# Kernel tuning notes

Measured on AMD Instinct MI355X. Metric: run time of the kernel, lower is better.

## Reference

```python
import jax, jax.numpy as jnp
import numpy as np
import math

B, S, HID = 4, 2048, 1024
H, D = 16, HID // 16


def setup_inputs() -> dict:
    key = jax.random.key(0)
    ks = jax.random.split(key, 6)
    scale = 0.02
    inp = {
        "hidden_states": jax.random.normal(ks[0], (B, S, HID), dtype=jnp.float32),
        "Wq": jax.random.normal(ks[1], (HID, HID), dtype=jnp.float32) * scale,
        "bq": jnp.zeros((HID,), dtype=jnp.float32),
        "Wk1": jax.random.normal(ks[2], (HID, HID), dtype=jnp.float32) * scale,
        "bk1": jnp.zeros((HID,), dtype=jnp.float32),
        "Wk2": jax.random.normal(ks[3], (HID, HID), dtype=jnp.float32) * scale,
        "bk2": jnp.zeros((HID,), dtype=jnp.float32),
        "Wv1": jax.random.normal(ks[4], (HID, HID), dtype=jnp.float32) * scale,
        "bv1": jnp.zeros((HID,), dtype=jnp.float32),
        "Wv2": jax.random.normal(ks[5], (HID, HID), dtype=jnp.float32) * scale,
        "bv2": jnp.zeros((HID,), dtype=jnp.float32),
    }
    return inp


def _heads(x):
    # [B, S, HID] -> [B, H, S, D]
    return x.reshape(B, S, H, D).transpose(0, 2, 1, 3)


def reference(hidden_states, Wq, bq, Wk1, bk1, Wk2, bk2, Wv1, bv1, Wv2, bv2):
    # nn.Linear uses y = x @ W^T + b
    q = _heads(hidden_states @ Wq.T + bq)
    k1 = _heads(hidden_states @ Wk1.T + bk1)
    k2 = _heads(hidden_states @ Wk2.T + bk2)
    v1 = _heads(hidden_states @ Wv1.T + bv1)
    v2 = _heads(hidden_states @ Wv2.T + bv2)

    inv_sqrt_d = 1.0 / math.sqrt(D)
    scores = jnp.einsum('bhqd,bhkd->bhqk', q, k1) * inv_sqrt_d  # [B,H,S,S]
    probs = jax.nn.softmax(scores, axis=-1)
    ctx = jnp.einsum('bhqk,bhkd->bhqd', probs, v1)              # [B,H,S,D]
    ctx = jnp.einsum('bhqd,bhkd->bhqk', ctx, k2)                # [B,H,S,S]
    ctx = jnp.einsum('bhqk,bhkd->bhqd', ctx, v2)                # [B,H,S,D]
    # [B,H,S,D] -> [B,S,HID]
    return ctx.transpose(0, 2, 1, 3).reshape(B, S, HID)
```

## Files before the change

### kernel.cpp

```cpp
#include <hip/hip_runtime.h>
#include <hip/hip_bf16.h>

#define HIDD 1024
#define BATCH 4
#define SEQ 2048
#define NHEAD 16
#define HD 64
#define NW 5
#define MROWS (BATCH*SEQ)
#define NCOLS (NW*HIDD)

typedef __attribute__((ext_vector_type(8))) short bf16x8;
typedef __attribute__((ext_vector_type(4))) float f32x4;
typedef __attribute__((ext_vector_type(16))) float f32x16;
typedef __attribute__((ext_vector_type(4))) unsigned int uint4v;

__device__ __forceinline__ unsigned short f2b(float f) {
    __hip_bfloat16 h = __float2bfloat16(f);
    return __builtin_bit_cast(unsigned short, h);
}
__device__ __forceinline__ float b2f(unsigned short u) {
    __hip_bfloat16 h = __builtin_bit_cast(__hip_bfloat16, u);
    return __bfloat162float(h);
}

#if __has_builtin(__builtin_amdgcn_exp2f)
#define EXP2(x) __builtin_amdgcn_exp2f(x)
#else
#define EXP2(x) exp2f(x)
#endif

typedef __attribute__((address_space(1))) const void gvoid;
typedef __attribute__((address_space(3))) void lvoid;
__device__ __forceinline__ void gload16(const void* src, void* dst) {
    __builtin_amdgcn_global_load_lds((gvoid*)src, (lvoid*)dst, 16, 0, 0);
}

__global__ void cvt_kernel(const float* __restrict__ X,
                           const float* __restrict__ W0, const float* __restrict__ W1,
                           const float* __restrict__ W2, const float* __restrict__ W3,
                           const float* __restrict__ W4,
                           unsigned short* __restrict__ Xb, unsigned short* __restrict__ Wb)
{
    const int XN = MROWS * HIDD / 4;
    const int WN = HIDD * HIDD / 4;
    int i = blockIdx.x * 256 + threadIdx.x;
    if (i >= XN + 5 * WN) return;
    const float* src; unsigned short* dst; int off;
    if (i < XN) { src = X; dst = Xb; off = i; }
    else {
        int j = i - XN; int w = j / WN; int r = j - w * WN;
        src = (w == 0 ? W0 : w == 1 ? W1 : w == 2 ? W2 : w == 3 ? W3 : W4);
        dst = Wb + (long)w * HIDD * HIDD; off = r;
    }
    float4 v = ((const float4*)src)[off];
    short4 o;
    o.x = (short)f2b(v.x); o.y = (short)f2b(v.y);
    o.z = (short)f2b(v.z); o.w = (short)f2b(v.w);
    ((short4*)dst)[off] = o;
}

#define READ_A(buf, kh, mh) \
    _Pragma("unroll") \
    for (int mt = 0; mt < 4; ++mt) \
        af[mt] = *(const bf16x8*)((const char*)As[buf][kh] + \
                  (wr * 128 + (mh) * 64 + mt * 16 + q) * 64 + ((g ^ csw) << 4));
#define READ_B(buf, kh) \
    _Pragma("unroll") \
    for (int nt = 0; nt < 4; ++nt) \
        bfr[nt] = *(const bf16x8*)((const char*)Bs[buf][kh] + \
                  (wc * 64 + nt * 16 + q) * 64 + ((g ^ csw) << 4));
#define MFMA_Q(mh) \
    asm volatile("s_waitcnt lgkmcnt(0)" ::: "memory"); \
    __builtin_amdgcn_sched_barrier(0); \
    __builtin_amdgcn_s_setprio(1); \
    _Pragma("unroll") \
    for (int mt = 0; mt < 4; ++mt) \
    _Pragma("unroll") \
    for (int nt = 0; nt < 4; ++nt) \
        acc[(mh) * 4 + mt][nt] = __builtin_amdgcn_mfma_f32_16x16x32_bf16( \
            af[mt], bfr[nt], acc[(mh) * 4 + mt][nt], 0, 0, 0); \
    __builtin_amdgcn_s_setprio(0);

__global__ __launch_bounds__(512, 2) void gemm_proj(
    const unsigned short* __restrict__ Xb, const unsigned short* __restrict__ Wb,
    const float* __restrict__ pb0, const float* __restrict__ pb1, const float* __restrict__ pb2,
    const float* __restrict__ pb3, const float* __restrict__ pb4,
    unsigned short* __restrict__ C)
{
    __shared__ __align__(16) unsigned short As[2][2][256 * 32];
    __shared__ __align__(16) unsigned short Bs[2][2][256 * 32];
    int tid = threadIdx.x;
    int n = blockIdx.x;
    int xcd = n & 7, op = n >> 3;
    int ntile = (op < 16) ? 2 : 1;
    int lane = tid & 63, w = tid >> 6;
    int wr = w >> 2, wc = w & 3;
    int q = lane & 15, g = lane >> 4;
    int csw = (q >> 1) & 3;
    int srow = tid >> 2;
    int scol = ((tid & 3) ^ ((tid >> 3) & 3)) * 8;

    for (int tix = 0; tix < ntile; ++tix) {
        int o = op + tix * 64;
        int bm = xcd * 4 + (o & 3);
        int bn = o >> 2;

        if (tix) { asm volatile("s_barrier" ::: "memory"); }

        f32x4 acc[8][4] = {};
        const unsigned short* Ag = Xb + (long)(bm * 256) * HIDD;
        const unsigned short* Bg = Wb + (long)(bn * 256) * HIDD;

        auto stage = [&](const unsigned short* G, unsigned short* slot, int kc) {
#pragma unroll
            for (int l = 0; l < 2; ++l)
                gload16(G + (long)(l * 128 + srow) * HIDD + kc + scol,
                        (char*)slot + (l * 512 + tid) * 16);
        };

        stage(Ag, As[0][0], 0);
        stage(Bg, Bs[0][0], 0);
        stage(Ag, As[0][1], 32);
        stage(Bg, Bs[0][1], 32);
        stage(Ag, As[1][0], 64);
        stage(Bg, Bs[1][0], 64);

        for (int t = 0; t < 16; ++t) {
            int buf = t & 1;
            int kc1 = ((t + 1) & 15) * 64;
            int kc2 = ((t + 2) & 15) * 64;
            bf16x8 af[4], bfr[4];
            asm volatile("s_waitcnt vmcnt(8)" ::: "memory");
            asm volatile("s_barrier" ::: "memory");
            READ_A(buf, 0, 0)
            READ_B(buf, 0)
            stage(Ag, As[buf ^ 1][1], kc1 + 32);
            MFMA_Q(0)
            READ_A(buf, 0, 1)
            stage(Bg, Bs[buf ^ 1][1], kc1 + 32);
            MFMA_Q(1)
            asm volatile("s_waitcnt vmcnt(8)" ::: "memory");
            asm volatile("s_barrier" ::: "memory");
            READ_A(buf, 1, 0)
            READ_B(buf, 1)
            stage(Ag, As[buf][0], kc2);
            MFMA_Q(0)
            READ_A(buf, 1, 1)
            stage(Bg, Bs[buf][0], kc2);
            MFMA_Q(1)
        }

        int ncol0 = bn * 256 + wc * 64 + q;
        const float* bp = (bn < 4 ? pb0 : bn < 8 ? pb1 : bn < 12 ? pb2 : bn < 16 ? pb3 : pb4);
#pragma unroll
        for (int nt = 0; nt < 4; ++nt) {
            int ncol = ncol0 + nt * 16;
            float bv = bp[ncol & 1023];
#pragma unroll
            for (int mt = 0; mt < 8; ++mt) {
                int row = bm * 256 + wr * 128 + mt * 16 + g * 4;
#pragma unroll
                for (int r = 0; r < 4; ++r)
                    C[(long)(row + r) * NCOLS + ncol] = f2b(acc[mt][nt][r] + bv);
            }
        }
    }
}

#define QSCALE 0.180336880f
#define LDV 72
#define NT (SEQ / 64)

__global__ __launch_bounds__(512, 2) void flash1(
    const unsigned short* __restrict__ C, unsigned short* __restrict__ ctx)
{
    __shared__ unsigned short Ks[2][64 * 64];
    __shared__ unsigned short Vs[2][64 * LDV];
    __shared__ float Lbuf[8][32];
    int tid = threadIdx.x;
    int lane = tid & 63, w = tid >> 6;
    int q32 = lane & 31, hi = lane >> 5;
    int n = blockIdx.x;
    int qt = (n >> 3) & 7;
    int bh = (n & 7) * 8 + (n >> 6);
    int b = bh >> 4, h = bh & 15;
    long rowbase = (long)(b * SEQ) * NCOLS;
    int s0 = qt * 256;

    const unsigned short* Kg = C + rowbase + 1 * HIDD + h * 64;
    const unsigned short* Vg = C + rowbase + 3 * HIDD + h * 64;

    int krlo = lane >> 3;
    int kch  = (lane & 7) ^ krlo;
    int kp = tid & 31, dc = tid >> 5;
    int rsw = q32 & 7;

    bf16x8 qreg[4];
    {
        const unsigned short* Qp = C + rowbase + (long)(s0 + w * 32 + q32) * NCOLS + h * 64;
#pragma unroll
        for (int s = 0; s < 4; ++s) {
            bf16x8 v = *(const bf16x8*)(Qp + s * 16 + hi * 8);
#pragma unroll
            for (int j = 0; j < 8; j++)
                v[j] = (short)f2b(b2f((unsigned short)v[j]) * QSCALE);
            qreg[s] = v;
        }
    }

    gload16(Kg + (long)(w * 8 + krlo) * NCOLS + kch * 8,
            (char*)Ks[0] + w * 1024 + (lane << 4));
    if (tid < 256) {
        const unsigned short* vsrc = Vg + (long)(2 * kp) * NCOLS + dc * 8;
        bf16x8 v0 = *(const bf16x8*)vsrc;
        bf16x8 v1 = *(const bf16x8*)(vsrc + NCOLS);
        unsigned int* VsW = (unsigned int*)Vs[0];
#pragma unroll
        for (int j = 0; j < 8; j++) {
            unsigned int pk = ((unsigned int)(unsigned short)v0[j]) |
                              (((unsigned int)(unsigned short)v1[j]) << 16);
            VsW[(dc * 8 + j) * (LDV / 2) + kp] = pk;
        }
    }
    __syncthreads();

    f32x16 O0 = {}, O1 = {};
    float l_run = 0.f;

    auto body = [&](int kt, int cur, int nxt) {
        int ktn = (kt + 1) & (NT - 1);
        gload16(Kg + (long)(ktn * 64 + w * 8 + krlo) * NCOLS + kch * 8,
                (char*)Ks[nxt] + w * 1024 + (lane << 4));
        bf16x8 nv0 = {}, nv1 = {};
        if (tid < 256) {
            const unsigned short* nsrc = Vg + (long)(ktn * 64 + 2 * kp) * NCOLS + dc * 8;
            nv0 = *(const bf16x8*)nsrc;
            nv1 = *(const bf16x8*)(nsrc + NCOLS);
        }

        float lsum = 0.f;
        __builtin_amdgcn_s_setprio(1);
#pragma unroll
        for (int kb = 0; kb < 2; ++kb) {
            f32x16 st = {};
#pragma unroll
            for (int s = 0; s < 4; ++s) {
                bf16x8 kf = *(const bf16x8*)((const char*)Ks[cur] +
                             ((kb * 32 + q32) << 7) + (((2 * s + hi) ^ rsw) << 4));
                st = __builtin_amdgcn_mfma_f32_32x32x16_bf16(kf, qreg[s], st, 0, 0, 0);
            }
            float e[16];
#pragma unroll
            for (int r = 0; r < 16; ++r) e[r] = EXP2(st[r]);
            lsum += (((e[0]+e[1])+(e[2]+e[3])) + ((e[4]+e[5])+(e[6]+e[7])))
                  + (((e[8]+e[9])+(e[10]+e[11])) + ((e[12]+e[13])+(e[14]+e[15])));
            unsigned int Cw[8];
#pragma unroll
            for (int p = 0; p < 8; ++p)
                asm("v_cvt_pk_bf16_f32 %0, %1, %2" : "=v"(Cw[p]) : "v"(e[2*p]), "v"(e[2*p+1]));
#pragma unroll
            for (int t2 = 0; t2 < 2; ++t2) {
                unsigned int a0 = Cw[t2*4+0], a1 = Cw[t2*4+1];
                unsigned int a2 = Cw[t2*4+2], a3 = Cw[t2*4+3];
                asm("v_permlane32_swap_b32 %0, %1" : "+v"(a0), "+v"(a2));
                asm("v_permlane32_swap_b32 %0, %1" : "+v"(a1), "+v"(a3));
                uint4v aw; aw[0] = a0; aw[1] = a1; aw[2] = a2; aw[3] = a3;
                bf16x8 af = __builtin_bit_cast(bf16x8, aw);
                int t = kb * 2 + t2;
#pragma unroll
                for (int nt = 0; nt < 2; ++nt) {
                    bf16x8 vf = *(const bf16x8*)((const char*)Vs[cur] +
                                 (nt * 32 + q32) * (LDV * 2) + t * 32 + hi * 16);
                    if (nt == 0) O0 = __builtin_amdgcn_mfma_f32_32x32x16_bf16(af, vf, O0, 0, 0, 0);
                    else         O1 = __builtin_amdgcn_mfma_f32_32x32x16_bf16(af, vf, O1, 0, 0, 0);
                }
            }
        }
        __builtin_amdgcn_s_setprio(0);
        l_run += lsum;
        if (tid < 256) {
            unsigned int* VsWn = (unsigned int*)Vs[nxt];
#pragma unroll
            for (int j = 0; j < 8; ++j) {
                unsigned int pk = ((unsigned int)(unsigned short)nv0[j]) |
                                  (((unsigned int)(unsigned short)nv1[j]) << 16);
                VsWn[(dc * 8 + j) * (LDV / 2) + kp] = pk;
            }
        }
        __syncthreads();
    };

    for (int kt = 0; kt < NT; kt += 2) {
        body(kt, 0, 1);
        body(kt + 1, 1, 0);
    }

    l_run += __shfl_xor(l_run, 32);
    float linv = 1.f / l_run;
    Lbuf[w][q32] = linv;
    asm volatile("s_waitcnt lgkmcnt(0)" ::: "memory");
#pragma unroll
    for (int reg = 0; reg < 16; ++reg) {
        int row = (reg & 3) + 8 * (reg >> 2) + 4 * hi;
        float lr = Lbuf[w][row];
        unsigned short* dst = ctx + ((long)bh * SEQ + s0 + w * 32 + row) * 64 + q32;
        dst[0]  = f2b(O0[reg] * lr);
        dst[32] = f2b(O1[reg] * lr);
    }
}

#define LDT2 72
__global__ __launch_bounds__(256) void m_partial(
    const unsigned short* __restrict__ C, float* __restrict__ part)
{
    __shared__ unsigned short Kt[64 * LDT2];
    __shared__ unsigned short Vt[64 * LDT2];
    int tid = threadIdx.x;
    int lane = tid & 63, w = tid >> 6;
    int q32 = lane & 31, hi = lane >> 5;
    int sc = blockIdx.x;
    int bh = blockIdx.y; int b = bh >> 4, h = bh & 15;
    const unsigned short* K2 = C + (long)(b * SEQ) * NCOLS + 2 * HIDD + h * 64;
    const unsigned short* V2 = C + (long)(b * SEQ) * NCOLS + 4 * HIDD + h * 64;
    int kp = tid & 31, dc = tid >> 5;
    int d2h = w >> 1, d1h = w & 1;
    unsigned int* KtW = (unsigned int*)Kt;
    unsigned int* VtW = (unsigned int*)Vt;
    f32x16 acc = {};

    for (int tk = 0; tk < 4; ++tk) {
        int sbase = sc * 256 + tk * 64;
        if (tk) __syncthreads();
        const unsigned short* ks = K2 + (long)(sbase + 2 * kp) * NCOLS + dc * 8;
        bf16x8 k0 = *(const bf16x8*)ks, k1 = *(const bf16x8*)(ks + NCOLS);
        const unsigned short* vs = V2 + (long)(sbase + 2 * kp) * NCOLS + dc * 8;
        bf16x8 v0 = *(const bf16x8*)vs, v1 = *(const bf16x8*)(vs + NCOLS);
#pragma unroll
        for (int j = 0; j < 8; ++j) {
            KtW[(dc * 8 + j) * (LDT2 / 2) + kp] =
                (unsigned int)(unsigned short)k0[j] | ((unsigned int)(unsigned short)k1[j] << 16);
            VtW[(dc * 8 + j) * (LDT2 / 2) + kp] =
                (unsigned int)(unsigned short)v0[j] | ((unsigned int)(unsigned short)v1[j] << 16);
        }
        __syncthreads();
#pragma unroll
        for (int t = 0; t < 4; ++t) {
            bf16x8 afr = *(const bf16x8*)(Vt + (d2h * 32 + q32) * LDT2 + t * 16 + hi * 8);
            bf16x8 bfr = *(const bf16x8*)(Kt + (d1h * 32 + q32) * LDT2 + t * 16 + hi * 8);
            acc = __builtin_amdgcn_mfma_f32_32x32x16_bf16(afr, bfr, acc, 0, 0, 0);
        }
    }
    float* dst = part + ((long)(sc * 64 + bh) << 12);
#pragma unroll
    for (int reg = 0; reg < 16; ++reg) {
        int d2 = d2h * 32 + (reg & 3) + 8 * (reg >> 2) + 4 * hi;
        dst[d2 * 64 + d1h * 32 + q32] = acc[reg];
    }
}

__global__ void m_reduce(const float* __restrict__ part, float* __restrict__ MT)
{
    int i = blockIdx.x * 256 + threadIdx.x;
    if (i >= 64 * 4096) return;
    int bh = i >> 12, e = i & 4095;
    float s = 0.f;
#pragma unroll
    for (int sc = 0; sc < 8; sc++) s += part[((long)(sc * 64 + bh) << 12) + e];
    MT[i] = s;
}

#define LDF 72
#define LDM 68
__global__ __launch_bounds__(256) void final_out(
    const unsigned short* __restrict__ ctx, const float* __restrict__ MT,
    float* __restrict__ out)
{
    __shared__ unsigned short cs[64 * LDF];
    __shared__ float msT[64 * LDM];
    int tid = threadIdx.x;
    int st0 = blockIdx.x * 4;
    int bh = blockIdx.y; int b = bh >> 4, h = bh & 15;
    {
        const float* Msrc = MT + ((long)bh << 12);
        for (int i = tid; i < 4096; i += 256)
            msT[(i & 63) * LDM + (i >> 6)] = Msrc[i];
    }
    int s4 = (tid & 15) * 4, j4 = (tid >> 4) * 4;
    for (int ti = 0; ti < 4; ++ti) {
        int st = st0 + ti;
        if (ti) __syncthreads();
        {
            int i = tid >> 2, dcx = tid & 3;
            const unsigned short* src = ctx + ((long)bh * SEQ + st * 64 + i) * 64 + dcx * 16;
            *(int4*)(cs + i * LDF + dcx * 16)     = *(const int4*)src;
            *(int4*)(cs + i * LDF + dcx * 16 + 8) = *(const int4*)(src + 8);
        }
        __syncthreads();
        f32x4 acc[4] = {};
        for (int d1b = 0; d1b < 8; ++d1b) {
            bf16x8 cv[4];
#pragma unroll
            for (int r = 0; r < 4; ++r)
                cv[r] = *(const bf16x8*)(cs + (s4 + r) * LDF + d1b * 8);
#pragma unroll
            for (int dd = 0; dd < 8; ++dd) {
                f32x4 mj = *(const f32x4*)(msT + (d1b * 8 + dd) * LDM + j4);
#pragma unroll
                for (int r = 0; r < 4; ++r) {
                    float c = b2f((unsigned short)cv[r][dd]);
#pragma unroll
                    for (int j = 0; j < 4; ++j)
                        acc[r][j] += c * mj[j];
                }
            }
        }
        float* dst0 = out + (long)(b * SEQ + st * 64) * HIDD + h * 64;
#pragma unroll
        for (int r = 0; r < 4; ++r)
            *(f32x4*)(dst0 + (long)(s4 + r) * HIDD + j4) = acc[r];
    }
}

extern "C" void kernel_launch(void* const* d_in, const int* in_sizes, int n_in,
                              void* d_out, int out_size, void* d_ws, size_t ws_size,
                              hipStream_t stream)
{
    const float* X   = (const float*)d_in[0];
    const float* Wq  = (const float*)d_in[1];
    const float* bq  = (const float*)d_in[2];
    const float* Wk1 = (const float*)d_in[3];
    const float* bk1 = (const float*)d_in[4];
    const float* Wk2 = (const float*)d_in[5];
    const float* bk2 = (const float*)d_in[6];
    const float* Wv1 = (const float*)d_in[7];
    const float* bv1 = (const float*)d_in[8];
    const float* Wv2 = (const float*)d_in[9];
    const float* bv2 = (const float*)d_in[10];

    char* ws = (char*)d_ws;
    unsigned short* Xb  = (unsigned short*)(ws);
    unsigned short* Wb  = (unsigned short*)(ws + 16777216);
    unsigned short* C   = (unsigned short*)(ws + 27262976);
    unsigned short* ctx = (unsigned short*)(ws + 111149056);
    float* part         = (float*)(ws + 127926272);
    float* MT           = (float*)(ws + 136314880);
    float* out = (float*)d_out;

    cvt_kernel<<<dim3(13312), 256, 0, stream>>>(X, Wq, Wk1, Wk2, Wv1, Wv2, Xb, Wb);
    gemm_proj<<<dim3(512), 512, 0, stream>>>(Xb, Wb, bq, bk1, bk2, bv1, bv2, C);
    flash1<<<dim3(512), 512, 0, stream>>>(C, ctx);
    m_partial<<<dim3(8, 64), 256, 0, stream>>>(C, part);
    m_reduce<<<dim3(1024), 256, 0, stream>>>(part, MT);
    final_out<<<dim3(8, 64), 256, 0, stream>>>(ctx, MT, out);
}
```

Baseline: 244.9 us.

## Restructure projection GEMM main loop to one barrier per K-step with staggered halves

Replaces the fine-grained interleaved pipeline, which used two barriers per 64-wide K step and partial vmcnt waits, with a simpler scheme. Each iteration waits for all loads, issues the full next-step prefetch into the other buffer, then runs both K halves with all fragments loaded before the MFMAs. Odd and even waves process the halves in opposite order to spread LDS bank pressure. This halves the number of barriers, but waiting on vmcnt(0) exposes global load latency, holding 12 fragments raises register pressure, and the explicit scheduling barriers are gone.

```diff
diff --git a/kernel.cpp b/kernel.cpp
--- a/kernel.cpp
+++ b/kernel.cpp
@@ -59,28 +59,6 @@
     o.z = (short)f2b(v.z); o.w = (short)f2b(v.w);
     ((short4*)dst)[off] = o;
 }
-
-#define READ_A(buf, kh, mh) \
-    _Pragma("unroll") \
-    for (int mt = 0; mt < 4; ++mt) \
-        af[mt] = *(const bf16x8*)((const char*)As[buf][kh] + \
-                  (wr * 128 + (mh) * 64 + mt * 16 + q) * 64 + ((g ^ csw) << 4));
-#define READ_B(buf, kh) \
-    _Pragma("unroll") \
-    for (int nt = 0; nt < 4; ++nt) \
-        bfr[nt] = *(const bf16x8*)((const char*)Bs[buf][kh] + \
-                  (wc * 64 + nt * 16 + q) * 64 + ((g ^ csw) << 4));
-#define MFMA_Q(mh) \
-    asm volatile("s_waitcnt lgkmcnt(0)" ::: "memory"); \
-    __builtin_amdgcn_sched_barrier(0); \
-    __builtin_amdgcn_s_setprio(1); \
-    _Pragma("unroll") \
-    for (int mt = 0; mt < 4; ++mt) \
-    _Pragma("unroll") \
-    for (int nt = 0; nt < 4; ++nt) \
-        acc[(mh) * 4 + mt][nt] = __builtin_amdgcn_mfma_f32_16x16x32_bf16( \
-            af[mt], bfr[nt], acc[(mh) * 4 + mt][nt], 0, 0, 0); \
-    __builtin_amdgcn_s_setprio(0);
 
 __global__ __launch_bounds__(512, 2) void gemm_proj(
     const unsigned short* __restrict__ Xb, const unsigned short* __restrict__ Wb,
@@ -119,36 +97,53 @@
                         (char*)slot + (l * 512 + tid) * 16);
         };
 
+        auto half = [&](int buf, int kh) {
+            bf16x8 b0[4], a0[4], a1[4];
+#pragma unroll
+            for (int nt = 0; nt < 4; ++nt)
+                b0[nt] = *(const bf16x8*)((const char*)Bs[buf][kh] +
+                          (wc * 64 + nt * 16 + q) * 64 + ((g ^ csw) << 4));
+#pragma unroll
+            for (int mt = 0; mt < 4; ++mt)
+                a0[mt] = *(const bf16x8*)((const char*)As[buf][kh] +
+                          (wr * 128 + mt * 16 + q) * 64 + ((g ^ csw) << 4));
+#pragma unroll
+            for (int mt = 0; mt < 4; ++mt)
+                a1[mt] = *(const bf16x8*)((const char*)As[buf][kh] +
+                          (wr * 128 + 64 + mt * 16 + q) * 64 + ((g ^ csw) << 4));
+            __builtin_amdgcn_s_setprio(1);
+#pragma unroll
+            for (int mt = 0; mt < 4; ++mt)
+#pragma unroll
+                for (int nt = 0; nt < 4; ++nt)
+                    acc[mt][nt] = __builtin_amdgcn_mfma_f32_16x16x32_bf16(
+                        a0[mt], b0[nt], acc[mt][nt], 0, 0, 0);
+#pragma unroll
+            for (int mt = 0; mt < 4; ++mt)
+#pragma unroll
+                for (int nt = 0; nt < 4; ++nt)
+                    acc[4 + mt][nt] = __builtin_amdgcn_mfma_f32_16x16x32_bf16(
+                        a1[mt], b0[nt], acc[4 + mt][nt], 0, 0, 0);
+            __builtin_amdgcn_s_setprio(0);
+        };
+
         stage(Ag, As[0][0], 0);
         stage(Bg, Bs[0][0], 0);
         stage(Ag, As[0][1], 32);
         stage(Bg, Bs[0][1], 32);
-        stage(Ag, As[1][0], 64);
-        stage(Bg, Bs[1][0], 64);
 
         for (int t = 0; t < 16; ++t) {
             int buf = t & 1;
-            int kc1 = ((t + 1) & 15) * 64;
-            int kc2 = ((t + 2) & 15) * 64;
-            bf16x8 af[4], bfr[4];
-            asm volatile("s_waitcnt vmcnt(8)" ::: "memory");
+            int kcn = ((t + 1) & 15) * 64;
+            asm volatile("s_waitcnt vmcnt(0)" ::: "memory");
             asm volatile("s_barrier" ::: "memory");
-            READ_A(buf, 0, 0)
-            READ_B(buf, 0)
-            stage(Ag, As[buf ^ 1][1], kc1 + 32);
-            MFMA_Q(0)
-            READ_A(buf, 0, 1)
-            stage(Bg, Bs[buf ^ 1][1], kc1 + 32);
-            MFMA_Q(1)
-            asm volatile("s_waitcnt vmcnt(8)" ::: "memory");
-            asm volatile("s_barrier" ::: "memory");
-            READ_A(buf, 1, 0)
-            READ_B(buf, 1)
-            stage(Ag, As[buf][0], kc2);
-            MFMA_Q(0)
-            READ_A(buf, 1, 1)
-            stage(Bg, Bs[buf][0], kc2);
-            MFMA_Q(1)
+            stage(Ag, As[buf ^ 1][0], kcn);
+            stage(Bg, Bs[buf ^ 1][0], kcn);
+            stage(Ag, As[buf ^ 1][1], kcn + 32);
+            stage(Bg, Bs[buf ^ 1][1], kcn + 32);
+            if ((w & 1) == 0) { half(buf, 0); half(buf, 1); }
+            else              { half(buf, 1); half(buf, 0); }
+            asm volatile("s_waitcnt lgkmcnt(0)" ::: "memory");
         }
 
         int ncol0 = bn * 256 + wc * 64 + q;
```

Result: slower. 253.2 us (+3.4%).
